# Kernel optimization log

Hardware: AMD Instinct MI355X
Metric: run time of the kernel (lower is better)

The kernel has to match this reference:

```python
import jax, jax.numpy as jnp
import numpy as np

NORM = 20.0   # from dataset 'NETS'
ALPHA = 1.0
EPS = 1e-12   # torch F.normalize eps


def _l2_normalize(x):
    n = jnp.sqrt(jnp.sum(x * x, axis=-1, keepdims=True))
    return x / jnp.maximum(n, EPS)


def setup_inputs() -> dict:
    key = jax.random.key(0)
    k1, k2, k3, k4, k5 = jax.random.split(key, 5)
    B, P, C = 4096, 32, 512
    predicted_score = jax.random.uniform(k1, (B,), dtype=jnp.float32) * NORM
    targets = jax.random.uniform(k2, (B,), dtype=jnp.float32) * NORM
    feats = jax.random.normal(k3, (B, C), dtype=jnp.float32)
    pivot_features = jax.random.normal(k4, (B, P, C), dtype=jnp.float32)
    pivot_scores = jax.random.uniform(k5, (B, P), dtype=jnp.float32) * NORM
    return {
        "predicted_score": predicted_score,
        "targets": targets,
        "feats": feats,
        "pivot_features": pivot_features,
        "pivot_scores": pivot_scores,
    }


def reference(predicted_score, targets, feats, pivot_features, pivot_scores):
    scale = ALPHA * NORM
    f = _l2_normalize(feats)                      # (B, C)
    pf = _l2_normalize(pivot_features)            # (B, P, C)
    ps = pivot_scores.astype(jnp.float32)         # (B, P)

    # image-text: (B,1,C) @ (B,C,P) -> (B,P)
    it_matches = jnp.einsum('bc,bpc->bp', f, pf)
    it_label = 1.0 - 2.0 * jnp.abs(targets[:, None] - ps) / scale
    image_text_loss = jnp.mean(jnp.abs(it_matches - it_label))

    # image-image: (B,B)
    ii_matches = f @ f.T
    ii_label = 1.0 - 2.0 * jnp.abs(targets[:, None] - targets[None, :]) / scale
    image_image_loss = jnp.mean(jnp.abs(ii_matches - ii_label))

    # text-text: (B,P,P)
    tt_matches = jnp.einsum('bpc,bqc->bpq', pf, pf)
    tt_label = 1.0 - 2.0 * jnp.abs(ps[:, :, None] - ps[:, None, :]) / scale
    text_text_loss = jnp.mean(jnp.abs(tt_matches - tt_label))

    mae_loss = jnp.mean(jnp.abs(predicted_score - targets))

    return (image_image_loss, text_text_loss, image_text_loss, mae_loss)
```

## Files before the change

### kernel.cpp

```cpp
#include <hip/hip_runtime.h>
#include <hip/hip_bf16.h>
#include <stdint.h>

#define B_N 4096
#define P_N 32
#define C_N 512
#define LABC 0.1f
#define N_II 528
#define GRID_TOTAL (N_II * 9)
#define N_TTSLOT (GRID_TOTAL - N_II)

typedef float  floatx4 __attribute__((ext_vector_type(4)));
typedef __bf16 bf16x8  __attribute__((ext_vector_type(8)));

__device__ __forceinline__ unsigned short f2bf(float x) {
    return __builtin_bit_cast(unsigned short, __float2bfloat16(x));
}
__device__ __forceinline__ uint4 pack8(const float4& v0, const float4& v1) {
    uint4 pk;
    pk.x = (unsigned)f2bf(v0.x) | ((unsigned)f2bf(v0.y) << 16);
    pk.y = (unsigned)f2bf(v0.z) | ((unsigned)f2bf(v0.w) << 16);
    pk.z = (unsigned)f2bf(v1.x) | ((unsigned)f2bf(v1.y) << 16);
    pk.w = (unsigned)f2bf(v1.z) | ((unsigned)f2bf(v1.w) << 16);
    return pk;
}
__device__ __forceinline__ void bfly_reduce2(float& a, float& b) {
#pragma unroll
    for (int m = 1; m < 64; m <<= 1) {
        a += __shfl_xor(a, m, 64);
        b += __shfl_xor(b, m, 64);
    }
}
__device__ __forceinline__ void bfly_reduce1(float& a) {
#pragma unroll
    for (int m = 1; m < 64; m <<= 1) a += __shfl_xor(a, m, 64);
}

__global__ __launch_bounds__(256) void k_prep(const float* __restrict__ feats,
                                              const float* __restrict__ pred,
                                              const float* __restrict__ targ,
                                              unsigned short* __restrict__ fb,
                                              float* __restrict__ maePart) {
    const int wave = threadIdx.x >> 6, lane = threadIdx.x & 63;
    const int row = blockIdx.x * 4 + wave;
    const float* src = feats + (size_t)row * C_N + lane * 8;
    float4 v0 = *(const float4*)src;
    float4 v1 = *(const float4*)(src + 4);
    float ss = v0.x*v0.x + v0.y*v0.y + v0.z*v0.z + v0.w*v0.w
             + v1.x*v1.x + v1.y*v1.y + v1.z*v1.z + v1.w*v1.w;
    bfly_reduce1(ss);
    const float inv = rsqrtf(fmaxf(ss, 1e-24f));
    float4 n0 = {v0.x*inv, v0.y*inv, v0.z*inv, v0.w*inv};
    float4 n1 = {v1.x*inv, v1.y*inv, v1.z*inv, v1.w*inv};
    *(uint4*)(fb + (size_t)row * C_N + lane * 8) = pack8(n0, n1);

    if (wave == 0) {
        float v = 0.f;
        if (lane < 4) {
            const int r = blockIdx.x * 4 + lane;
            v = fabsf(pred[r] - targ[r]);
        }
        v += __shfl_xor(v, 1, 64);
        v += __shfl_xor(v, 2, 64);
        if (lane == 0) maePart[blockIdx.x] = v;
    }
}

#define APAD 130
struct TTsm {
    float psS[P_N];
    float rdiag[P_N];
    float redT[4], redI[4];
};
struct IIsm {
    unsigned short As[4 * APAD * 8];
    unsigned short Bs[4 * APAD * 8];
    float tm[128], tn[128];
    float red[4];
};
union SMu { TTsm tt; IIsm ii; };

__global__ __launch_bounds__(256) void k_fused(const float* __restrict__ pf_g,
                                               const float* __restrict__ ps_g,
                                               const float* __restrict__ targets,
                                               const unsigned short* __restrict__ fb,
                                               double* __restrict__ partII,
                                               double* __restrict__ partTT,
                                               double* __restrict__ partIT) {
    __shared__ __align__(16) SMu sm;
    const int tid = threadIdx.x, wave = tid >> 6, lane = tid & 63;
    const int quad = lane >> 4, l15 = lane & 15;
    const int bid = blockIdx.x;
    const bool isII = (bid % 9) == 0;

    if (isII) {
        IIsm& S = sm.ii;
        int bm = 0, rem = bid / 9;
        while (rem >= 32 - bm) { rem -= 32 - bm; ++bm; }
        const int bn = bm + rem;
        const int wr = wave >> 1, wc = wave & 1;
        const int mbase = bm * 128, nbase = bn * 128;

        if (tid < 128) S.tm[tid] = targets[mbase + tid];
        else           S.tn[tid - 128] = targets[nbase + tid - 128];

        const int row = tid >> 1, half = tid & 1;
        const unsigned short* aSrc = fb + (size_t)(mbase + row) * C_N + half * 16;
        const unsigned short* bSrc = fb + (size_t)(nbase + row) * C_N + half * 16;
        const int c0 = half * 2, c1 = half * 2 + 1;

        floatx4 accv[16];
#pragma unroll
        for (int i = 0; i < 16; ++i) accv[i] = (floatx4){0.f, 0.f, 0.f, 0.f};

        uint4 a0 = *(const uint4*)(aSrc);
        uint4 a1 = *(const uint4*)(aSrc + 8);
        uint4 b0 = *(const uint4*)(bSrc);
        uint4 b1 = *(const uint4*)(bSrc + 8);

        for (int ks = 0; ks < 16; ++ks) {
            __syncthreads();
            *(uint4*)&S.As[((size_t)c0 * APAD + row) * 8] = a0;
            *(uint4*)&S.As[((size_t)c1 * APAD + row) * 8] = a1;
            *(uint4*)&S.Bs[((size_t)c0 * APAD + row) * 8] = b0;
            *(uint4*)&S.Bs[((size_t)c1 * APAD + row) * 8] = b1;
            __syncthreads();
            if (ks < 15) {
                const int off = (ks + 1) * 32;
                a0 = *(const uint4*)(aSrc + off);
                a1 = *(const uint4*)(aSrc + off + 8);
                b0 = *(const uint4*)(bSrc + off);
                b1 = *(const uint4*)(bSrc + off + 8);
            }
            bf16x8 af[4], bfv[4];
#pragma unroll
            for (int t = 0; t < 4; ++t)
                af[t] = __builtin_bit_cast(bf16x8, *(const uint4*)&S.As[((size_t)quad * APAD + wr * 64 + t * 16 + l15) * 8]);
#pragma unroll
            for (int t = 0; t < 4; ++t)
                bfv[t] = __builtin_bit_cast(bf16x8, *(const uint4*)&S.Bs[((size_t)quad * APAD + wc * 64 + t * 16 + l15) * 8]);
#pragma unroll
            for (int ti = 0; ti < 4; ++ti)
#pragma unroll
                for (int tj = 0; tj < 4; ++tj)
                    accv[ti * 4 + tj] = __builtin_amdgcn_mfma_f32_16x16x32_bf16(af[ti], bfv[tj], accv[ti * 4 + tj], 0, 0, 0);
        }

        float s = 0.f;
#pragma unroll
        for (int ti = 0; ti < 4; ++ti)
#pragma unroll
            for (int tj = 0; tj < 4; ++tj)
#pragma unroll
                for (int r = 0; r < 4; ++r) {
                    const int p = wr * 64 + ti * 16 + quad * 4 + r;
                    const int q = wc * 64 + tj * 16 + l15;
                    const float lab = 1.f - LABC * fabsf(S.tm[p] - S.tn[q]);
                    s += fabsf(accv[ti * 4 + tj][r] - lab);
                }
        if (bm != bn) s *= 2.f;
        bfly_reduce1(s);
        if (lane == 0) S.red[wave] = s;
        __syncthreads();
        if (tid == 0) partII[bid / 9] = (double)(S.red[0] + S.red[1] + S.red[2] + S.red[3]);
    } else {
        const int b = bid - (bid / 9) - 1;
        TTsm& S = sm.tt;
        if (b >= B_N) {
            if (tid == 0) { partTT[b] = 0.0; partIT[b] = 0.0; }
            return;
        }

        if (tid < P_N) S.psS[tid] = ps_g[b * P_N + tid];
        const float tb = targets[b];

        const int pt = (wave >> 1) * 16, qt = (wave & 1) * 16;
        const bool doF = (wave < 2);

        const float* rowA = pf_g + (size_t)b * P_N * C_N + (size_t)(pt + l15) * C_N;
        const float* rowB = pf_g + (size_t)b * P_N * C_N + (size_t)(qt + l15) * C_N;
        const unsigned short* fbrow = fb + (size_t)b * C_N;

        floatx4 acc4 = {0.f, 0.f, 0.f, 0.f};
        floatx4 accF = {0.f, 0.f, 0.f, 0.f};
        const uint4 zero4 = {0u, 0u, 0u, 0u};
#pragma unroll
        for (int kk = 0; kk < 16; ++kk) {
            const int off = kk * 32 + quad * 8;
            const float4 a0 = *(const float4*)(rowA + off);
            const float4 a1 = *(const float4*)(rowA + off + 4);
            const float4 b0 = *(const float4*)(rowB + off);
            const float4 b1 = *(const float4*)(rowB + off + 4);
            const bf16x8 afrag = __builtin_bit_cast(bf16x8, pack8(a0, a1));
            const bf16x8 bfrag = __builtin_bit_cast(bf16x8, pack8(b0, b1));
            acc4 = __builtin_amdgcn_mfma_f32_16x16x32_bf16(afrag, bfrag, acc4, 0, 0, 0);
            if (doF) {
                const uint4 fr = *(const uint4*)(fbrow + off);
                const bf16x8 af = __builtin_bit_cast(bf16x8, (l15 == 0) ? fr : zero4);
                accF = __builtin_amdgcn_mfma_f32_16x16x32_bf16(af, bfrag, accF, 0, 0, 0);
            }
        }
        if (pt == qt) {
            if ((l15 >> 2) == quad) S.rdiag[pt + l15] = rsqrtf(fmaxf(acc4[l15 & 3], 1e-24f));
        }
        __syncthreads();

        float tt_sum = 0.f, it_sum = 0.f;
#pragma unroll
        for (int r = 0; r < 4; ++r) {
            const int p = pt + quad * 4 + r;
            const int q = qt + l15;
            const float val = acc4[r] * S.rdiag[p] * S.rdiag[q];
            const float lab = 1.f - LABC * fabsf(S.psS[p] - S.psS[q]);
            tt_sum += fabsf(val - lab);
        }
        if (doF && quad == 0) {
            const int q = qt + l15;
            const float val = accF[0] * S.rdiag[q];
            const float lab = 1.f - LABC * fabsf(tb - S.psS[q]);
            it_sum = fabsf(val - lab);
        }
        bfly_reduce2(tt_sum, it_sum);
        if (lane == 0) { S.redT[wave] = tt_sum; S.redI[wave] = it_sum; }
        __syncthreads();
        if (tid == 0) {
            partTT[b] = (double)(S.redT[0] + S.redT[1] + S.redT[2] + S.redT[3]);
            partIT[b] = (double)(S.redI[0] + S.redI[1] + S.redI[2] + S.redI[3]);
        }
    }
}

__global__ __launch_bounds__(256) void k_final(const double* __restrict__ partII,
                                               const double* __restrict__ partTT,
                                               const double* __restrict__ partIT,
                                               const float* __restrict__ maePart,
                                               float* __restrict__ out) {
    __shared__ double redA[4], redB[4], redC[4];
    __shared__ float redM[4];
    const int tid = threadIdx.x, wave = tid >> 6, lane = tid & 63;

    double sII = 0.0, sTT = 0.0, sIT = 0.0;
    for (int i = tid; i < N_II; i += 256) sII += partII[i];
    for (int i = tid; i < N_TTSLOT; i += 256) { sTT += partTT[i]; sIT += partIT[i]; }
    float sM = maePart[tid] + maePart[tid + 256] + maePart[tid + 512] + maePart[tid + 768];

#pragma unroll
    for (int m = 1; m < 64; m <<= 1) {
        sII += __shfl_xor(sII, m, 64);
        sTT += __shfl_xor(sTT, m, 64);
        sIT += __shfl_xor(sIT, m, 64);
        sM  += __shfl_xor(sM, m, 64);
    }
    if (lane == 0) { redA[wave] = sII; redB[wave] = sTT; redC[wave] = sIT; redM[wave] = sM; }
    __syncthreads();
    if (tid == 0) {
        const double ii = redA[0] + redA[1] + redA[2] + redA[3];
        const double tt = redB[0] + redB[1] + redB[2] + redB[3];
        const double it = redC[0] + redC[1] + redC[2] + redC[3];
        out[0] = (float)(ii / (double)((size_t)B_N * B_N));
        out[1] = (float)(tt / (double)((size_t)B_N * P_N * P_N));
        out[2] = (float)(it / (double)((size_t)B_N * P_N));
        out[3] = (redM[0] + redM[1] + redM[2] + redM[3]) * (1.f / B_N);
    }
}

extern "C" void kernel_launch(void* const* d_in, const int* in_sizes, int n_in,
                              void* d_out, int out_size, void* d_ws, size_t ws_size,
                              hipStream_t stream) {
    const float* pred  = (const float*)d_in[0];
    const float* targ  = (const float*)d_in[1];
    const float* feats = (const float*)d_in[2];
    const float* pf    = (const float*)d_in[3];
    const float* ps    = (const float*)d_in[4];
    float* out = (float*)d_out;

    float* maePart      = (float*)d_ws;
    double* partII      = (double*)((char*)d_ws + 4096);
    double* partTT      = (double*)((char*)d_ws + 16384);
    double* partIT      = (double*)((char*)d_ws + 65536);
    unsigned short* fb  = (unsigned short*)((char*)d_ws + 131072);

    k_prep<<<B_N / 4, 256, 0, stream>>>(feats, pred, targ, fb, maePart);
    k_fused<<<GRID_TOTAL, 256, 0, stream>>>(pf, ps, targ, fb, partII, partTT, partIT);
    k_final<<<1, 256, 0, stream>>>(partII, partTT, partIT, maePart, out);
}
```

Measured before the change: 469.0 us.

## Split TT Gram matrix over K across waves with shared-memory reduction

Each wave now loads a 128-wide K slice of all 32 pivot rows once and computes the full 32x32 Gram tile plus the feature row with six MFMAs per step. Partial results are summed across the four waves in LDS. Previously each wave computed one 16x16 quadrant over the full K, so every pivot row was loaded twice. The change halves global loads of pivot features and issues all loads up front for more memory parallelism. In exchange it adds about 17KB of LDS per block, an extra barrier and a reduction, and sets launch bounds to 4 blocks per CU.

```diff
diff --git a/kernel.cpp b/kernel.cpp
--- a/kernel.cpp
+++ b/kernel.cpp
@@ -68,6 +68,8 @@
 
 #define APAD 130
 struct TTsm {
+    float part[4][32][33];
+    float partF[4][32];
     float psS[P_N];
     float rdiag[P_N];
     float redT[4], redI[4];
@@ -80,13 +82,13 @@
 };
 union SMu { TTsm tt; IIsm ii; };
 
-__global__ __launch_bounds__(256) void k_fused(const float* __restrict__ pf_g,
-                                               const float* __restrict__ ps_g,
-                                               const float* __restrict__ targets,
-                                               const unsigned short* __restrict__ fb,
-                                               double* __restrict__ partII,
-                                               double* __restrict__ partTT,
-                                               double* __restrict__ partIT) {
+__global__ __launch_bounds__(256, 4) void k_fused(const float* __restrict__ pf_g,
+                                                  const float* __restrict__ ps_g,
+                                                  const float* __restrict__ targets,
+                                                  const unsigned short* __restrict__ fb,
+                                                  double* __restrict__ partII,
+                                                  double* __restrict__ partTT,
+                                                  double* __restrict__ partIT) {
     __shared__ __align__(16) SMu sm;
     const int tid = threadIdx.x, wave = tid >> 6, lane = tid & 63;
     const int quad = lane >> 4, l15 = lane & 15;
@@ -174,50 +176,77 @@
         if (tid < P_N) S.psS[tid] = ps_g[b * P_N + tid];
         const float tb = targets[b];
 
-        const int pt = (wave >> 1) * 16, qt = (wave & 1) * 16;
-        const bool doF = (wave < 2);
-
-        const float* rowA = pf_g + (size_t)b * P_N * C_N + (size_t)(pt + l15) * C_N;
-        const float* rowB = pf_g + (size_t)b * P_N * C_N + (size_t)(qt + l15) * C_N;
-        const unsigned short* fbrow = fb + (size_t)b * C_N;
-
-        floatx4 acc4 = {0.f, 0.f, 0.f, 0.f};
-        floatx4 accF = {0.f, 0.f, 0.f, 0.f};
+        const float* rowLo = pf_g + (size_t)b * P_N * C_N + (size_t)l15 * C_N + wave * 128 + quad * 8;
+        const float* rowHi = rowLo + 16 * C_N;
+        float4 lo[4][2], hi[4][2];
+#pragma unroll
+        for (int kk = 0; kk < 4; ++kk) {
+            lo[kk][0] = *(const float4*)(rowLo + kk * 32);
+            lo[kk][1] = *(const float4*)(rowLo + kk * 32 + 4);
+        }
+#pragma unroll
+        for (int kk = 0; kk < 4; ++kk) {
+            hi[kk][0] = *(const float4*)(rowHi + kk * 32);
+            hi[kk][1] = *(const float4*)(rowHi + kk * 32 + 4);
+        }
         const uint4 zero4 = {0u, 0u, 0u, 0u};
-#pragma unroll
-        for (int kk = 0; kk < 16; ++kk) {
-            const int off = kk * 32 + quad * 8;
-            const float4 a0 = *(const float4*)(rowA + off);
-            const float4 a1 = *(const float4*)(rowA + off + 4);
-            const float4 b0 = *(const float4*)(rowB + off);
-            const float4 b1 = *(const float4*)(rowB + off + 4);
-            const bf16x8 afrag = __builtin_bit_cast(bf16x8, pack8(a0, a1));
-            const bf16x8 bfrag = __builtin_bit_cast(bf16x8, pack8(b0, b1));
-            acc4 = __builtin_amdgcn_mfma_f32_16x16x32_bf16(afrag, bfrag, acc4, 0, 0, 0);
-            if (doF) {
-                const uint4 fr = *(const uint4*)(fbrow + off);
-                const bf16x8 af = __builtin_bit_cast(bf16x8, (l15 == 0) ? fr : zero4);
-                accF = __builtin_amdgcn_mfma_f32_16x16x32_bf16(af, bfrag, accF, 0, 0, 0);
-            }
-        }
-        if (pt == qt) {
-            if ((l15 >> 2) == quad) S.rdiag[pt + l15] = rsqrtf(fmaxf(acc4[l15 & 3], 1e-24f));
-        }
+        uint4 fq[4] = {zero4, zero4, zero4, zero4};
+        if (l15 == 0) {
+            const unsigned short* fp = fb + (size_t)b * C_N + wave * 128 + quad * 8;
+#pragma unroll
+            for (int kk = 0; kk < 4; ++kk) fq[kk] = *(const uint4*)(fp + kk * 32);
+        }
+
+        floatx4 a00 = {0.f,0.f,0.f,0.f}, a01 = a00, a10 = a00, a11 = a00, f0 = a00, f1 = a00;
+#pragma unroll
+        for (int kk = 0; kk < 4; ++kk) {
+            const bf16x8 aL = __builtin_bit_cast(bf16x8, pack8(lo[kk][0], lo[kk][1]));
+            const bf16x8 aH = __builtin_bit_cast(bf16x8, pack8(hi[kk][0], hi[kk][1]));
+            a00 = __builtin_amdgcn_mfma_f32_16x16x32_bf16(aL, aL, a00, 0, 0, 0);
+            a01 = __builtin_amdgcn_mfma_f32_16x16x32_bf16(aL, aH, a01, 0, 0, 0);
+            a10 = __builtin_amdgcn_mfma_f32_16x16x32_bf16(aH, aL, a10, 0, 0, 0);
+            a11 = __builtin_amdgcn_mfma_f32_16x16x32_bf16(aH, aH, a11, 0, 0, 0);
+            const bf16x8 af = __builtin_bit_cast(bf16x8, fq[kk]);
+            f0 = __builtin_amdgcn_mfma_f32_16x16x32_bf16(af, aL, f0, 0, 0, 0);
+            f1 = __builtin_amdgcn_mfma_f32_16x16x32_bf16(af, aH, f1, 0, 0, 0);
+        }
+
+        float (*P)[33] = S.part[wave];
+#pragma unroll
+        for (int r = 0; r < 4; ++r) {
+            const int pr = quad * 4 + r;
+            P[pr][l15]           = a00[r];
+            P[pr][16 + l15]      = a01[r];
+            P[16 + pr][l15]      = a10[r];
+            P[16 + pr][16 + l15] = a11[r];
+        }
+        if (quad == 0) { S.partF[wave][l15] = f0[0]; S.partF[wave][16 + l15] = f1[0]; }
         __syncthreads();
 
+        float cell[4]; int cp[4], cq[4];
+#pragma unroll
+        for (int i = 0; i < 4; ++i) {
+            const int c = tid + i * 256;
+            const int p = c >> 5, qc = c & 31;
+            const float v = S.part[0][p][qc] + S.part[1][p][qc]
+                          + S.part[2][p][qc] + S.part[3][p][qc];
+            cell[i] = v; cp[i] = p; cq[i] = qc;
+            if (p == qc) S.rdiag[p] = rsqrtf(fmaxf(v, 1e-24f));
+        }
+        __syncthreads();
+
         float tt_sum = 0.f, it_sum = 0.f;
 #pragma unroll
-        for (int r = 0; r < 4; ++r) {
-            const int p = pt + quad * 4 + r;
-            const int q = qt + l15;
-            const float val = acc4[r] * S.rdiag[p] * S.rdiag[q];
-            const float lab = 1.f - LABC * fabsf(S.psS[p] - S.psS[q]);
+        for (int i = 0; i < 4; ++i) {
+            const float val = cell[i] * S.rdiag[cp[i]] * S.rdiag[cq[i]];
+            const float lab = 1.f - LABC * fabsf(S.psS[cp[i]] - S.psS[cq[i]]);
             tt_sum += fabsf(val - lab);
         }
-        if (doF && quad == 0) {
-            const int q = qt + l15;
-            const float val = accF[0] * S.rdiag[q];
-            const float lab = 1.f - LABC * fabsf(tb - S.psS[q]);
+        if (tid < P_N) {
+            const float fs = S.partF[0][tid] + S.partF[1][tid]
+                           + S.partF[2][tid] + S.partF[3][tid];
+            const float val = fs * S.rdiag[tid];
+            const float lab = 1.f - LABC * fabsf(tb - S.psS[tid]);
             it_sum = fabsf(val - lab);
         }
         bfly_reduce2(tt_sum, it_sum);
```

After: 387.2 us. 17.4% less time.
